# Performance work log

Hardware: AMD Instinct MI355X
Metric: run time of the kernel (lower is better)

The kernel has to match this reference:

```python
import jax, jax.numpy as jnp
import numpy as np

B, N = 128, 64
HID, MLP, DS, DV = 128, 128, 32, 32
DH = MLP - DS - DV  # 64
FILL = -10.0


def _embed_mask(x, W, b, fill):
    # Linear+ReLU on non-NaN rows; fill NaN rows with `fill` (matches embed_with_masking).
    nan = jnp.isnan(x).any(-1)
    e = jax.nn.relu(jnp.where(jnp.isnan(x), 0.0, x) @ W + b)
    return jnp.where(nan[..., None], jnp.asarray(fill, x.dtype), e)


def setup_inputs() -> dict:
    key = jax.random.key(0)
    ks = jax.random.split(key, 12)
    s = 0.05
    return {
        "hidden_states": jax.random.normal(ks[0], (B, N, HID), jnp.float32),
        "obs1": jax.random.normal(ks[1], (B, N, 2), jnp.float32),
        "obs2": jax.random.normal(ks[2], (B, N, 2), jnp.float32),
        "w_sp": jax.random.normal(ks[3], (2, DS), jnp.float32) * s,
        "b_sp": jnp.zeros((DS,), jnp.float32),
        "w_vel": jax.random.normal(ks[4], (2, DV), jnp.float32) * s,
        "b_vel": jnp.zeros((DV,), jnp.float32),
        "w_hid": jax.random.normal(ks[5], (HID, DH), jnp.float32) * s,
        "b_hid": jnp.zeros((DH,), jnp.float32),
        "wq": jax.random.normal(ks[6], (MLP, MLP), jnp.float32) * s,
        "wk": jax.random.normal(ks[7], (MLP, MLP), jnp.float32) * s,
        "wv": jax.random.normal(ks[8], (MLP, MLP), jnp.float32) * s,
        "in_proj_w": jax.random.normal(ks[9], (MLP, 3 * MLP), jnp.float32) * s,
        "in_proj_b": jnp.zeros((3 * MLP,), jnp.float32),
        "mha_out_w": jax.random.normal(ks[10], (MLP, MLP), jnp.float32) * s,
        "mha_out_b": jnp.zeros((MLP,), jnp.float32),
        "out_w": jax.random.normal(ks[11], (MLP, MLP), jnp.float32) * s,
        "out_b": jnp.zeros((MLP,), jnp.float32),
    }


def reference(hidden_states, obs1, obs2, w_sp, b_sp, w_vel, b_vel, w_hid, b_hid,
              wq, wk, wv, in_proj_w, in_proj_b, mha_out_w, mha_out_b, out_w, out_b):
    b, n = obs2.shape[0], obs2.shape[1]
    # relative positions: rel[b,i,j] = obs2[b,j] - obs2[b,i]
    rel = obs2[:, None, :, :] - obs2[:, :, None, :]              # [B,N,N,2]
    sp = _embed_mask(rel, w_sp, b_sp, FILL)                      # [B,N,N,DS]
    hid = _embed_mask(hidden_states, w_hid, b_hid, 0.0)          # [B,N,DH]
    hid_unf = jnp.broadcast_to(hid[:, None, :, :], (b, n, n, DH))
    vel = obs2 - obs1
    relvel = vel[:, None, :, :] - vel[:, :, None, :]             # [B,N,N,2]
    dv = _embed_mask(relvel * 4, w_vel, b_vel, FILL)             # [B,N,N,DV]
    emb = jnp.concatenate([sp, hid_unf, dv], axis=-1)            # [B,N,N,MLP]

    # MHA (1 head) in-proj weights split (stored as [in,out])
    w_iq, w_ik, w_iv = in_proj_w[:, :MLP], in_proj_w[:, MLP:2 * MLP], in_proj_w[:, 2 * MLP:]
    b_iq, b_ik, b_iv = in_proj_b[:MLP], in_proj_b[MLP:2 * MLP], in_proj_b[2 * MLP:]

    # Only the diagonal query position is kept by the final eye-mask gather,
    # and softmax rows are independent, so compute q only at j == i.
    idx = jnp.arange(n)
    emb_diag = emb[:, idx, idx]                                  # [B,N,MLP]
    q = (emb_diag @ wq) @ w_iq + b_iq                            # [B,N,MLP]
    k = (emb @ wk) @ w_ik + b_ik                                 # [B,N,N,MLP]
    v = (emb @ wv) @ w_iv + b_iv                                 # [B,N,N,MLP]

    scores = jnp.einsum('bid,bijd->bij', q, k) / jnp.sqrt(jnp.asarray(MLP, q.dtype))
    attn = jax.nn.softmax(scores, axis=-1)                       # [B,N,N]
    ctx = jnp.einsum('bij,bijd->bid', attn, v)                   # [B,N,MLP]
    mha_out = ctx @ mha_out_w + mha_out_b
    out = mha_out @ out_w + out_b                                # [B,N,out_dim]
    return out.reshape(b * n, -1)
```

## Files before the change

kernel.cpp:

```cpp
#include <hip/hip_runtime.h>

typedef float v2f __attribute__((ext_vector_type(2)));
typedef float v4f __attribute__((ext_vector_type(4)));
#define PKFMA(a,b,c) __builtin_elementwise_fma((a),(b),(c))
#define PKMAX(a,b)   __builtin_elementwise_max((a),(b))
static __device__ __forceinline__ v2f vsplat(float s) { return (v2f){s, s}; }
static __device__ __forceinline__ v4f v4splat(float s) { return (v4f){s, s, s, s}; }
static __device__ __forceinline__ v2f vmk(float a, float b) { return (v2f){a, b}; }
static __device__ __forceinline__ v2f shfl_xor_v2(v2f x, int m) {
    double d = __builtin_bit_cast(double, x);
    d = __shfl_xor(d, m, 64);
    return __builtin_bit_cast(v2f, d);
}
static __device__ __forceinline__ v2f red32_v2(v2f x) { return x + shfl_xor_v2(x, 32); }
static __device__ __forceinline__ v4f red32_v4(v4f x) {
    v2f lo = vmk(x.x, x.y), hi = vmk(x.z, x.w);
    lo = red32_v2(lo);  hi = red32_v2(hi);
    return (v4f){lo.x, lo.y, hi.x, hi.y};
}
static __device__ __forceinline__ float RL(float v, int lane) {
    return __builtin_bit_cast(float, __builtin_amdgcn_readlane(__builtin_bit_cast(int, v), lane));
}

#define WS_WQC   0
#define WS_WKC   16384
#define WS_WVC   32768
#define WS_MOW   49152
#define WS_GQ    65536
#define WS_G0Q   73728
#define WS_FALL  73856
#define WS_FB    90240
#define WS_HID   90368
#define WS_NEED_HID_BYTES ((size_t)(90368 + 128*64*64) * 4)

__global__ __launch_bounds__(256) void precompute1(
    const float* __restrict__ wq, const float* __restrict__ wk,
    const float* __restrict__ wv, const float* __restrict__ in_proj_w,
    const float* __restrict__ mha_out_w, const float* __restrict__ out_w,
    const float* __restrict__ hs, const float* __restrict__ w_hid,
    const float* __restrict__ b_hid, float* __restrict__ ws)
{
    __shared__ __align__(16) float sbuf[4224];
    const int tid = threadIdx.x;

    if (blockIdx.x < 256) {
        const int mat  = blockIdx.x >> 6;
        const int rp   = blockIdx.x & 63;
        const int rsel = tid >> 7;
        const int col  = tid & 127;
        const int r    = 2 * rp + rsel;
        const float* A; const float* Bm; int ldb; float* C;
        if (mat == 0)      { A = wq;        Bm = in_proj_w;       ldb = 384; C = ws + WS_WQC; }
        else if (mat == 1) { A = wk;        Bm = in_proj_w + 128; ldb = 384; C = ws + WS_WKC; }
        else if (mat == 2) { A = wv;        Bm = in_proj_w + 256; ldb = 384; C = ws + WS_WVC; }
        else               { A = mha_out_w; Bm = out_w;           ldb = 128; C = ws + WS_MOW; }
        sbuf[tid] = A[r * 128 + col];
        __syncthreads();
        float acc = 0.f;
        #pragma unroll 8
        for (int d = 0; d < 128; ++d) acc = fmaf(sbuf[rsel * 128 + d], Bm[d * ldb + col], acc);
        C[r * 128 + col] = acc;
    } else {
        const int b2 = blockIdx.x - 256;
        const int b = b2 >> 1, half = b2 & 1;
        const float4* src = (const float4*)(hs + b * 8192 + half * 4096);
        for (int k = tid; k < 1024; k += 256) {
            const int row = k >> 5, c = k & 31;
            *(float4*)&sbuf[row * 132 + 4 * c] = src[k];
        }
        __syncthreads();
        const int ty = tid >> 4, tx = tid & 15;
        float a0c[4] = {0,0,0,0}, a1c[4] = {0,0,0,0};
        for (int d0 = 0; d0 < 128; d0 += 4) {
            const float4 a0 = *(const float4*)&sbuf[(2*ty+0)*132 + d0];
            const float4 a1 = *(const float4*)&sbuf[(2*ty+1)*132 + d0];
            const float* a0p = (const float*)&a0;
            const float* a1p = (const float*)&a1;
            #pragma unroll
            for (int dd = 0; dd < 4; ++dd) {
                const float4 w4 = *(const float4*)&w_hid[(d0+dd)*64 + 4*tx];
                a0c[0] = fmaf(a0p[dd], w4.x, a0c[0]); a0c[1] = fmaf(a0p[dd], w4.y, a0c[1]);
                a0c[2] = fmaf(a0p[dd], w4.z, a0c[2]); a0c[3] = fmaf(a0p[dd], w4.w, a0c[3]);
                a1c[0] = fmaf(a1p[dd], w4.x, a1c[0]); a1c[1] = fmaf(a1p[dd], w4.y, a1c[1]);
                a1c[2] = fmaf(a1p[dd], w4.z, a1c[2]); a1c[3] = fmaf(a1p[dd], w4.w, a1c[3]);
            }
        }
        const float4 bh = *(const float4*)&b_hid[4*tx];
        float* dst = ws + WS_HID + b * 4096 + (32*half + 2*ty) * 64 + 4*tx;
        *(float4*)dst        = make_float4(fmaxf(a0c[0]+bh.x,0.f), fmaxf(a0c[1]+bh.y,0.f),
                                           fmaxf(a0c[2]+bh.z,0.f), fmaxf(a0c[3]+bh.w,0.f));
        *(float4*)(dst + 64) = make_float4(fmaxf(a1c[0]+bh.x,0.f), fmaxf(a1c[1]+bh.y,0.f),
                                           fmaxf(a1c[2]+bh.z,0.f), fmaxf(a1c[3]+bh.w,0.f));
    }
}

__global__ __launch_bounds__(128) void precompute2(
    const float* __restrict__ b_sp, const float* __restrict__ b_vel,
    const float* __restrict__ in_proj_b, const float* __restrict__ mha_out_b,
    const float* __restrict__ out_w, const float* __restrict__ out_b,
    float* __restrict__ ws)
{
    const float* Wqc = ws + WS_WQC;
    const float* Wkc = ws + WS_WKC;
    const float* Wvc = ws + WS_WVC;
    const float* Mow = ws + WS_MOW;
    const int bid = blockIdx.x, tid = threadIdx.x;
    __shared__ __align__(16) float sa[128];

    if (bid < 64) {
        const int k = bid;
        sa[tid] = Wqc[(32 + k) * 128 + tid];
        __syncthreads();
        const int j = tid;
        const int pj = (j < 64) ? 32 + j : ((j < 96) ? j - 64 : j);
        const float* brow = Wkc + pj * 128;
        float acc = 0.f;
        #pragma unroll 8
        for (int d = 0; d < 128; d += 4) {
            const float4 a4 = *(const float4*)&sa[d];
            const float4 b4 = *(const float4*)&brow[d];
            acc = fmaf(a4.x, b4.x, fmaf(a4.y, b4.y, fmaf(a4.z, b4.z, fmaf(a4.w, b4.w, acc))));
        }
        ws[WS_GQ + k * 128 + j] = acc;
    } else if (bid < 192) {
        const int k2 = bid - 64;
        const int srcRow = (k2 < 32) ? k2 : ((k2 < 64) ? 96 + (k2 - 32) : 32 + (k2 - 64));
        sa[tid] = Wvc[srcRow * 128 + tid];
        __syncthreads();
        float acc = 0.f;
        #pragma unroll 8
        for (int m = 0; m < 128; ++m) acc = fmaf(sa[m], Mow[m * 128 + tid], acc);
        ws[WS_FALL + k2 * 128 + tid] = acc;
    } else if (bid == 192) {
        float acc = out_b[tid];
        #pragma unroll 8
        for (int m = 0; m < 128; ++m) {
            acc = fmaf(in_proj_b[256 + m], Mow[m * 128 + tid], acc);
            acc = fmaf(mha_out_b[m], out_w[m * 128 + tid], acc);
        }
        ws[WS_FB + tid] = acc;
    } else {
        float qc = in_proj_b[tid];
        #pragma unroll 4
        for (int s = 0; s < 32; ++s) {
            qc = fmaf(fmaxf(b_sp[s], 0.f),  Wqc[s * 128 + tid], qc);
            qc = fmaf(fmaxf(b_vel[s], 0.f), Wqc[(96 + s) * 128 + tid], qc);
        }
        sa[tid] = qc;
        __syncthreads();
        const int j = tid;
        const int pj = (j < 64) ? 32 + j : ((j < 96) ? j - 64 : j);
        const float* brow = Wkc + pj * 128;
        float acc = 0.f;
        #pragma unroll 8
        for (int d = 0; d < 128; d += 4) {
            const float4 a4 = *(const float4*)&sa[d];
            const float4 b4 = *(const float4*)&brow[d];
            acc = fmaf(a4.x, b4.x, fmaf(a4.y, b4.y, fmaf(a4.z, b4.z, fmaf(a4.w, b4.w, acc))));
        }
        ws[WS_G0Q + j] = acc;
    }
}

#define L_GQ   0
#define L_G0Q  8192
#define L_FALL 8320
#define L_FB   24704
#define L_HID  24832
#define L_OBS  29056
#define L_WV   29312
#define L_TOT  35456

template <bool HIDWS>
__global__ __launch_bounds__(1024) void attn_main(
    const float* __restrict__ hs, const float* __restrict__ obs1,
    const float* __restrict__ obs2,
    const float* __restrict__ w_sp, const float* __restrict__ b_sp,
    const float* __restrict__ w_vel, const float* __restrict__ b_vel,
    const float* __restrict__ w_hid, const float* __restrict__ b_hid,
    const float* __restrict__ ws, float* __restrict__ out)
{
    const int tid = threadIdx.x;
    const int l   = tid & 63;
    const int w   = tid >> 6;
    const int b   = blockIdx.x >> 1;
    const int rg0 = (blockIdx.x & 1) * 32 + 2 * w;

    __shared__ __align__(16) float smem[L_TOT];
    float* const s_gq  = smem + L_GQ;
    float* const s_g0q = smem + L_G0Q;
    float* const s_fall= smem + L_FALL;
    float* const s_fb  = smem + L_FB;
    float* const s_hid = smem + L_HID;
    float* const s_obs = smem + L_OBS;
    float* const tt = smem + L_WV + w * 384;
    float* const qq = smem + L_WV + w * 384 + 128;
    float* const aa = smem + L_WV + w * 384 + 256;

    {
        const float4* src = (const float4*)(ws + WS_GQ);
        float4* dst = (float4*)smem;
        #pragma unroll
        for (int k = tid; k < 6208; k += 1024) dst[k] = src[k];
    }
    if (tid < 64) {
        const int g = b * 64 + tid;
        const float2 o2 = ((const float2*)obs2)[g];
        const float2 o1 = ((const float2*)obs1)[g];
        *(float4*)&s_obs[tid * 4] = make_float4(o2.x, o2.y, o2.x - o1.x, o2.y - o1.y);
    }
    if (HIDWS) {
        const float4* src = (const float4*)(ws + WS_HID + b * 4096);
        {
            const int k = tid;
            const int row = k >> 4, c4 = (k & 15) * 4;
            const float4 v = src[k];
            *(v2f*)&s_hid[row * 66 + c4]     = vmk(v.x, v.y);
            *(v2f*)&s_hid[row * 66 + c4 + 2] = vmk(v.z, v.w);
        }
    } else {
        const int r = tid >> 4, c0 = (tid & 15) * 4;
        float acc[4];
        #pragma unroll
        for (int c = 0; c < 4; ++c) acc[c] = b_hid[c0 + c];
        for (int k = 0; k < 128; ++k) {
            const float a = hs[b * 8192 + r * 128 + k];
            const float4 w4 = *(const float4*)&w_hid[k * 64 + c0];
            acc[0] = fmaf(a, w4.x, acc[0]);
            acc[1] = fmaf(a, w4.y, acc[1]);
            acc[2] = fmaf(a, w4.z, acc[2]);
            acc[3] = fmaf(a, w4.w, acc[3]);
        }
        *(v2f*)&s_hid[r * 66 + c0]     = vmk(fmaxf(acc[0], 0.f), fmaxf(acc[1], 0.f));
        *(v2f*)&s_hid[r * 66 + c0 + 2] = vmk(fmaxf(acc[2], 0.f), fmaxf(acc[3], 0.f));
    }
    __syncthreads();

    const int kh = l >> 5;
    const int cg = (l & 31) * 4;
    const int hsel = l >> 5;

    v4f rres;
    {
        v4f acc0 = {0,0,0,0}, acc1 = acc0;
        const int kb = 32 * kh;
        #pragma unroll
        for (int c8 = 0; c8 < 32; c8 += 8) {
            v2f h0[4], h1[4];
            #pragma unroll
            for (int j = 0; j < 4; ++j) {
                h0[j] = *(const v2f*)&s_hid[(rg0 + 0) * 66 + kb + c8 + 2 * j];
                h1[j] = *(const v2f*)&s_hid[(rg0 + 1) * 66 + kb + c8 + 2 * j];
            }
            #pragma unroll
            for (int j = 0; j < 4; ++j) {
                const int kk = kb + c8 + 2 * j;
                const v4f ga = *(const v4f*)&s_gq[kk * 128 + cg];
                const v4f gb = *(const v4f*)&s_gq[(kk + 1) * 128 + cg];
                acc0 = PKFMA(v4splat(h0[j].x), ga, PKFMA(v4splat(h0[j].y), gb, acc0));
                acc1 = PKFMA(v4splat(h1[j].x), ga, PKFMA(v4splat(h1[j].y), gb, acc1));
            }
        }
        acc0 = red32_v4(acc0);
        acc1 = red32_v4(acc1);
        const v4f bias = *(const v4f*)&s_g0q[cg];
        rres = (hsel ? acc1 : acc0) + bias;
    }

    float sc0, sc1;
    {
        v2f s0v = (v2f){0.f, 0.f}, s1v = s0v;
        const float* hl = &s_hid[l * 66];
        #pragma unroll
        for (int s = 0; s < 16; ++s) {
            const v2f hA = *(const v2f*)&hl[4 * s];
            const v2f hB = *(const v2f*)&hl[4 * s + 2];
            const v2f t0A = vmk(RL(rres.x, s),      RL(rres.y, s));
            const v2f t0B = vmk(RL(rres.z, s),      RL(rres.w, s));
            const v2f t1A = vmk(RL(rres.x, 32 + s), RL(rres.y, 32 + s));
            const v2f t1B = vmk(RL(rres.z, 32 + s), RL(rres.w, 32 + s));
            s0v = PKFMA(t0A, hA, PKFMA(t0B, hB, s0v));
            s1v = PKFMA(t1A, hA, PKFMA(t1B, hB, s1v));
        }
        sc0 = s0v.x + s0v.y;  sc1 = s1v.x + s1v.y;
    }

    v2f aa2;
    {
        const float4 oj  = *(const float4*)&s_obs[4 * l];
        const float4 oiA = *(const float4*)&s_obs[4 * (rg0 + 0)];
        const float4 oiB = *(const float4*)&s_obs[4 * (rg0 + 1)];
        const float rx0 = oj.x - oiA.x, ry0 = oj.y - oiA.y;
        const float dx0 = (oj.z - oiA.z) * 4.f, dy0 = (oj.w - oiA.w) * 4.f;
        const float rx1 = oj.x - oiB.x, ry1 = oj.y - oiB.y;
        const float dx1 = (oj.z - oiB.z) * 4.f, dy1 = (oj.w - oiB.w) * 4.f;
        v4f acc0 = {0,0,0,0}, acc1 = acc0;
        #pragma unroll
        for (int g = 0; g < 8; ++g) {
            const int s0 = 4 * g;
            const v4f w0p = *(const v4f*)&w_sp[s0];
            const v4f w1p = *(const v4f*)&w_sp[32 + s0];
            const v4f bsp = *(const v4f*)&b_sp[s0];
            const v4f u0p = *(const v4f*)&w_vel[s0];
            const v4f u1p = *(const v4f*)&w_vel[32 + s0];
            const v4f bvp = *(const v4f*)&b_vel[s0];
            const int lqs = 16 + g, lqd = 24 + g;
            const v4f q0s = {RL(rres.x, lqs), RL(rres.y, lqs), RL(rres.z, lqs), RL(rres.w, lqs)};
            const v4f q0d = {RL(rres.x, lqd), RL(rres.y, lqd), RL(rres.z, lqd), RL(rres.w, lqd)};
            const v4f q1s = {RL(rres.x, 32 + lqs), RL(rres.y, 32 + lqs),
                             RL(rres.z, 32 + lqs), RL(rres.w, 32 + lqs)};
            const v4f q1d = {RL(rres.x, 32 + lqd), RL(rres.y, 32 + lqd),
                             RL(rres.z, 32 + lqd), RL(rres.w, 32 + lqd)};
            const v4f esp0 = PKMAX(PKFMA(v4splat(rx0), w0p,
                                   PKFMA(v4splat(ry0), w1p, bsp)), v4splat(0.f));
            const v4f edv0 = PKMAX(PKFMA(v4splat(dx0), u0p,
                                   PKFMA(v4splat(dy0), u1p, bvp)), v4splat(0.f));
            acc0 = PKFMA(q0s, esp0, PKFMA(q0d, edv0, acc0));
            const v4f esp1 = PKMAX(PKFMA(v4splat(rx1), w0p,
                                   PKFMA(v4splat(ry1), w1p, bsp)), v4splat(0.f));
            const v4f edv1 = PKMAX(PKFMA(v4splat(dx1), u0p,
                                   PKFMA(v4splat(dy1), u1p, bvp)), v4splat(0.f));
            acc1 = PKFMA(q1s, esp1, PKFMA(q1d, edv1, acc1));
        }
        const float scale = 0.08838834764831845f;
        v2f p01 = vmk((sc0 + ((acc0.x + acc0.y) + (acc0.z + acc0.w))) * scale,
                      (sc1 + ((acc1.x + acc1.y) + (acc1.z + acc1.w))) * scale);
        v2f m01 = p01;
        #pragma unroll
        for (int off = 32; off > 0; off >>= 1)
            m01 = PKMAX(m01, shfl_xor_v2(m01, off));
        v2f e01 = vmk(__expf(p01.x - m01.x), __expf(p01.y - m01.y));
        v2f u01 = e01;
        #pragma unroll
        for (int off = 32; off > 0; off >>= 1)
            u01 = u01 + shfl_xor_v2(u01, off);
        aa2 = vmk(e01.x / u01.x, e01.y / u01.y);
        *(v2f*)&aa[2 * l] = aa2;
    }

    {
        const int jh = l >> 5, s = l & 31;
        const v2f wa = vmk(w_sp[s],      w_vel[s]);
        const v2f wb = vmk(w_sp[32 + s], w_vel[32 + s]);
        const v2f bb = vmk(b_sp[s],      b_vel[s]);
        const float4 oi0 = *(const float4*)&s_obs[4 * (rg0 + 0)];
        const float4 oi1 = *(const float4*)&s_obs[4 * (rg0 + 1)];
        v2f acc0 = (v2f){0.f, 0.f}, acc1 = acc0;
        const int j0 = 32 * jh;
        for (int j = j0; j < j0 + 32; ++j) {
            const v2f a2 = *(const v2f*)&aa[2 * j];
            const float4 o4 = *(const float4*)&s_obs[4 * j];
            {
                const v2f xx = vmk(o4.x - oi0.x, (o4.z - oi0.z) * 4.f);
                const v2f yy = vmk(o4.y - oi0.y, (o4.w - oi0.w) * 4.f);
                const v2f e2 = PKMAX(PKFMA(xx, wa, PKFMA(yy, wb, bb)), vsplat(0.f));
                acc0 = PKFMA(vsplat(a2.x), e2, acc0);
            }
            {
                const v2f xx = vmk(o4.x - oi1.x, (o4.z - oi1.z) * 4.f);
                const v2f yy = vmk(o4.y - oi1.y, (o4.w - oi1.w) * 4.f);
                const v2f e2 = PKMAX(PKFMA(xx, wa, PKFMA(yy, wb, bb)), vsplat(0.f));
                acc1 = PKFMA(vsplat(a2.y), e2, acc1);
            }
        }
        acc0 = red32_v2(acc0);
        acc1 = red32_v2(acc1);
        const v2f accw = jh ? acc1 : acc0;
        tt[jh * 64 + s]      = accw.x;
        tt[jh * 64 + 32 + s] = accw.y;
    }

    {
        v2f ah = (v2f){0.f, 0.f};
        #pragma unroll 8
        for (int j = 0; j < 64; ++j) {
            const v2f a2 = vmk(RL(aa2.x, j), RL(aa2.y, j));
            ah = PKFMA(a2, vsplat(s_hid[j * 66 + l]), ah);
        }
        qq[l] = ah.x;  qq[64 + l] = ah.y;
    }

    {
        const float* Asrc = kh ? qq : tt;
        v4f acc0 = {0,0,0,0}, acc1 = acc0;
        #pragma unroll
        for (int c8 = 0; c8 < 64; c8 += 8) {
            v2f a0[4], a1[4];
            #pragma unroll
            for (int j = 0; j < 4; ++j) {
                a0[j] = *(const v2f*)&Asrc[c8 + 2 * j];
                a1[j] = *(const v2f*)&Asrc[64 + c8 + 2 * j];
            }
            #pragma unroll
            for (int j = 0; j < 4; ++j) {
                const int kk = 64 * kh + c8 + 2 * j;
                const v4f fa = *(const v4f*)&s_fall[kk * 128 + cg];
                const v4f fc = *(const v4f*)&s_fall[(kk + 1) * 128 + cg];
                acc0 = PKFMA(v4splat(a0[j].x), fa, PKFMA(v4splat(a0[j].y), fc, acc0));
                acc1 = PKFMA(v4splat(a1[j].x), fa, PKFMA(v4splat(a1[j].y), fc, acc1));
            }
        }
        acc0 = red32_v4(acc0);
        acc1 = red32_v4(acc1);
        const v4f fb4 = *(const v4f*)&s_fb[cg];
        const v4f o = (hsel ? acc1 : acc0) + fb4;
        const int gr = (b * 64 + rg0 + hsel) * 128 + cg;
        *(v4f*)&out[gr] = o;
    }
}

extern "C" void kernel_launch(void* const* d_in, const int* in_sizes, int n_in,
                              void* d_out, int out_size, void* d_ws, size_t ws_size,
                              hipStream_t stream) {
    const float* hs        = (const float*)d_in[0];
    const float* obs1      = (const float*)d_in[1];
    const float* obs2      = (const float*)d_in[2];
    const float* w_sp      = (const float*)d_in[3];
    const float* b_sp      = (const float*)d_in[4];
    const float* w_vel     = (const float*)d_in[5];
    const float* b_vel     = (const float*)d_in[6];
    const float* w_hid     = (const float*)d_in[7];
    const float* b_hid     = (const float*)d_in[8];
    const float* wq        = (const float*)d_in[9];
    const float* wk        = (const float*)d_in[10];
    const float* wv        = (const float*)d_in[11];
    const float* in_proj_w = (const float*)d_in[12];
    const float* in_proj_b = (const float*)d_in[13];
    const float* mha_out_w = (const float*)d_in[14];
    const float* mha_out_b = (const float*)d_in[15];
    const float* out_w     = (const float*)d_in[16];
    const float* out_b     = (const float*)d_in[17];
    float* ws  = (float*)d_ws;
    float* out = (float*)d_out;

    const bool hidws = (ws_size >= WS_NEED_HID_BYTES);

    precompute1<<<hidws ? 512 : 256, 256, 0, stream>>>(
        wq, wk, wv, in_proj_w, mha_out_w, out_w, hs, w_hid, b_hid, ws);
    precompute2<<<194, 128, 0, stream>>>(
        b_sp, b_vel, in_proj_b, mha_out_b, out_w, out_b, ws);
    if (hidws) {
        attn_main<true><<<256, 1024, 0, stream>>>(hs, obs1, obs2, w_sp, b_sp, w_vel, b_vel,
                                                  w_hid, b_hid, ws, out);
    } else {
        attn_main<false><<<256, 1024, 0, stream>>>(hs, obs1, obs2, w_sp, b_sp, w_vel, b_vel,
                                                   w_hid, b_hid, ws, out);
    }
}
```

Before: 125.7 us.

## Split final output GEMM out of attention kernel into separate kernel

Moves the fused mha-out/out projection out of the attention kernel. The attention kernel now writes per-row partial activations to workspace, and a new 256-thread out_gemm kernel multiplies them by the combined weight matrix with a bias. This cuts the attention kernel's shared memory from about 141KB to about 59KB, so more blocks can be resident per CU. The cost is an extra kernel launch and a global write and read of an 8192x128 intermediate. The non-hidws path now also needs a larger workspace.

```diff
diff --git a/kernel.cpp b/kernel.cpp
--- a/kernel.cpp
+++ b/kernel.cpp
@@ -30,8 +30,9 @@
 #define WS_G0Q   73728
 #define WS_FALL  73856
 #define WS_FB    90240
-#define WS_HID   90368
-#define WS_NEED_HID_BYTES ((size_t)(90368 + 128*64*64) * 4)
+#define WS_PA    90368
+#define WS_HID   1138944
+#define WS_NEED_HID_BYTES ((size_t)(1138944 + 128*64*64) * 4)
 
 __global__ __launch_bounds__(256) void precompute1(
     const float* __restrict__ wq, const float* __restrict__ wk,
@@ -164,21 +165,19 @@
 
 #define L_GQ   0
 #define L_G0Q  8192
-#define L_FALL 8320
-#define L_FB   24704
-#define L_HID  24832
-#define L_OBS  29056
-#define L_WV   29312
-#define L_TOT  35456
+#define L_HID  8320
+#define L_OBS  12544
+#define L_AA   12800
+#define L_TOT  14848
 
 template <bool HIDWS>
-__global__ __launch_bounds__(1024) void attn_main(
+__global__ __launch_bounds__(1024) void attn_core(
     const float* __restrict__ hs, const float* __restrict__ obs1,
     const float* __restrict__ obs2,
     const float* __restrict__ w_sp, const float* __restrict__ b_sp,
     const float* __restrict__ w_vel, const float* __restrict__ b_vel,
     const float* __restrict__ w_hid, const float* __restrict__ b_hid,
-    const float* __restrict__ ws, float* __restrict__ out)
+    const float* __restrict__ ws, float* __restrict__ pa)
 {
     const int tid = threadIdx.x;
     const int l   = tid & 63;
@@ -189,19 +188,15 @@
     __shared__ __align__(16) float smem[L_TOT];
     float* const s_gq  = smem + L_GQ;
     float* const s_g0q = smem + L_G0Q;
-    float* const s_fall= smem + L_FALL;
-    float* const s_fb  = smem + L_FB;
     float* const s_hid = smem + L_HID;
     float* const s_obs = smem + L_OBS;
-    float* const tt = smem + L_WV + w * 384;
-    float* const qq = smem + L_WV + w * 384 + 128;
-    float* const aa = smem + L_WV + w * 384 + 256;
+    float* const aa = smem + L_AA + w * 128;
 
     {
         const float4* src = (const float4*)(ws + WS_GQ);
         float4* dst = (float4*)smem;
         #pragma unroll
-        for (int k = tid; k < 6208; k += 1024) dst[k] = src[k];
+        for (int k = tid; k < 2080; k += 1024) dst[k] = src[k];
     }
     if (tid < 64) {
         const int g = b * 64 + tid;
@@ -287,13 +282,13 @@
 
     v2f aa2;
     {
-        const float4 oj  = *(const float4*)&s_obs[4 * l];
+        const float4 oj4 = *(const float4*)&s_obs[4 * l];
         const float4 oiA = *(const float4*)&s_obs[4 * (rg0 + 0)];
         const float4 oiB = *(const float4*)&s_obs[4 * (rg0 + 1)];
-        const float rx0 = oj.x - oiA.x, ry0 = oj.y - oiA.y;
-        const float dx0 = (oj.z - oiA.z) * 4.f, dy0 = (oj.w - oiA.w) * 4.f;
-        const float rx1 = oj.x - oiB.x, ry1 = oj.y - oiB.y;
-        const float dx1 = (oj.z - oiB.z) * 4.f, dy1 = (oj.w - oiB.w) * 4.f;
+        const float rx0 = oj4.x - oiA.x, ry0 = oj4.y - oiA.y;
+        const float dx0 = (oj4.z - oiA.z) * 4.f, dy0 = (oj4.w - oiA.w) * 4.f;
+        const float rx1 = oj4.x - oiB.x, ry1 = oj4.y - oiB.y;
+        const float dx1 = (oj4.z - oiB.z) * 4.f, dy1 = (oj4.w - oiB.w) * 4.f;
         v4f acc0 = {0,0,0,0}, acc1 = acc0;
         #pragma unroll
         for (int g = 0; g < 8; ++g) {
@@ -366,8 +361,9 @@
         acc0 = red32_v2(acc0);
         acc1 = red32_v2(acc1);
         const v2f accw = jh ? acc1 : acc0;
-        tt[jh * 64 + s]      = accw.x;
-        tt[jh * 64 + 32 + s] = accw.y;
+        const int grow = (b * 64 + rg0 + jh) * 128;
+        pa[grow + s]      = accw.x;
+        pa[grow + 32 + s] = accw.y;
     }
 
     {
@@ -377,36 +373,58 @@
             const v2f a2 = vmk(RL(aa2.x, j), RL(aa2.y, j));
             ah = PKFMA(a2, vsplat(s_hid[j * 66 + l]), ah);
         }
-        qq[l] = ah.x;  qq[64 + l] = ah.y;
-    }
-
-    {
-        const float* Asrc = kh ? qq : tt;
-        v4f acc0 = {0,0,0,0}, acc1 = acc0;
-        #pragma unroll
-        for (int c8 = 0; c8 < 64; c8 += 8) {
-            v2f a0[4], a1[4];
+        const int grow = (b * 64 + rg0) * 128;
+        pa[grow + 64 + l]       = ah.x;
+        pa[grow + 128 + 64 + l] = ah.y;
+    }
+}
+
+__global__ __launch_bounds__(256) void out_gemm(
+    const float* __restrict__ ws, float* __restrict__ out)
+{
+    __shared__ __align__(16) float sF[16384 + 128 + 4096];
+    float* const sFall = sF;
+    float* const sfb   = sF + 16384;
+    float* const sA    = sF + 16512;
+    const int tid = threadIdx.x;
+    const int r0 = blockIdx.x * 32;
+    {
+        const float4* src = (const float4*)(ws + WS_FALL);
+        float4* dst = (float4*)sFall;
+        #pragma unroll
+        for (int k = tid; k < 4096; k += 256) dst[k] = src[k];
+    }
+    if (tid < 32) ((float4*)sfb)[tid] = ((const float4*)(ws + WS_FB))[tid];
+    {
+        const float4* src = (const float4*)(ws + WS_PA + r0 * 128);
+        float4* dst = (float4*)sA;
+        #pragma unroll
+        for (int k = tid; k < 1024; k += 256) dst[k] = src[k];
+    }
+    __syncthreads();
+
+    const int c2 = 2 * (tid & 63);
+    const int rg = (tid >> 6) * 8;
+    const v2f fb2 = *(const v2f*)&sfb[c2];
+    v2f acc[8];
+    #pragma unroll
+    for (int r = 0; r < 8; ++r) acc[r] = fb2;
+    for (int k = 0; k < 128; k += 4) {
+        v4f a[8];
+        #pragma unroll
+        for (int r = 0; r < 8; ++r) a[r] = *(const v4f*)&sA[(rg + r) * 128 + k];
+        #pragma unroll
+        for (int kk = 0; kk < 4; ++kk) {
+            const v2f f = *(const v2f*)&sFall[(k + kk) * 128 + c2];
             #pragma unroll
-            for (int j = 0; j < 4; ++j) {
-                a0[j] = *(const v2f*)&Asrc[c8 + 2 * j];
-                a1[j] = *(const v2f*)&Asrc[64 + c8 + 2 * j];
-            }
-            #pragma unroll
-            for (int j = 0; j < 4; ++j) {
-                const int kk = 64 * kh + c8 + 2 * j;
-                const v4f fa = *(const v4f*)&s_fall[kk * 128 + cg];
-                const v4f fc = *(const v4f*)&s_fall[(kk + 1) * 128 + cg];
-                acc0 = PKFMA(v4splat(a0[j].x), fa, PKFMA(v4splat(a0[j].y), fc, acc0));
-                acc1 = PKFMA(v4splat(a1[j].x), fa, PKFMA(v4splat(a1[j].y), fc, acc1));
-            }
-        }
-        acc0 = red32_v4(acc0);
-        acc1 = red32_v4(acc1);
-        const v4f fb4 = *(const v4f*)&s_fb[cg];
-        const v4f o = (hsel ? acc1 : acc0) + fb4;
-        const int gr = (b * 64 + rg0 + hsel) * 128 + cg;
-        *(v4f*)&out[gr] = o;
-    }
+            for (int r = 0; r < 8; ++r)
+                acc[r] = PKFMA(vsplat(a[r][kk]), f, acc[r]);
+        }
+    }
+    const int gbase = (r0 + rg) * 128 + c2;
+    #pragma unroll
+    for (int r = 0; r < 8; ++r)
+        *(v2f*)&out[gbase + r * 128] = acc[r];
 }
 
 extern "C" void kernel_launch(void* const* d_in, const int* in_sizes, int n_in,
@@ -440,10 +458,11 @@
     precompute2<<<194, 128, 0, stream>>>(
         b_sp, b_vel, in_proj_b, mha_out_b, out_w, out_b, ws);
     if (hidws) {
-        attn_main<true><<<256, 1024, 0, stream>>>(hs, obs1, obs2, w_sp, b_sp, w_vel, b_vel,
-                                                  w_hid, b_hid, ws, out);
+        attn_core<true><<<256, 1024, 0, stream>>>(hs, obs1, obs2, w_sp, b_sp, w_vel, b_vel,
+                                                  w_hid, b_hid, ws, ws + WS_PA);
     } else {
-        attn_main<false><<<256, 1024, 0, stream>>>(hs, obs1, obs2, w_sp, b_sp, w_vel, b_vel,
-                                                   w_hid, b_hid, ws, out);
-    }
-}
+        attn_core<false><<<256, 1024, 0, stream>>>(hs, obs1, obs2, w_sp, b_sp, w_vel, b_vel,
+                                                   w_hid, b_hid, ws, ws + WS_PA);
+    }
+    out_gemm<<<256, 256, 0, stream>>>(ws, out);
+}
```

Result: slower. 137.0 us (+9.0%).
